# Optimization experiments

Hardware: AMD Instinct MI355X
Metric: run time of the kernel (lower is better)

## Reference

```python
import jax, jax.numpy as jnp
import numpy as np

H = 64  # hidden_dim

def _gru_cell(x, h, Wih, Whh, bih, bhh):
    # PyTorch GRUCell math: gates ordered (r, z, n)
    gi = x @ Wih.T + bih            # [B, 3H]
    gh = h @ Whh.T + bhh            # [B, 3H]
    i_r, i_z, i_n = jnp.split(gi, 3, axis=-1)
    h_r, h_z, h_n = jnp.split(gh, 3, axis=-1)
    r = jax.nn.sigmoid(i_r + h_r)
    z = jax.nn.sigmoid(i_z + h_z)
    n = jnp.tanh(i_n + r * h_n)
    return (1.0 - z) * n + z * h

def setup_inputs() -> dict:
    key = jax.random.key(0)
    ks = jax.random.split(key, 13)
    B, T, D = 128, 512, 512
    x = jax.random.normal(ks[0], (B, T, D), dtype=jnp.float32)
    s = 1.0 / np.sqrt(H)
    def u(k, shape):
        return jax.random.uniform(k, shape, dtype=jnp.float32, minval=-s, maxval=s)
    return {
        "x": x,
        "W0ih": u(ks[1], (3 * H, D)), "W0hh": u(ks[2], (3 * H, H)),
        "b0ih": u(ks[3], (3 * H,)),   "b0hh": u(ks[4], (3 * H,)),
        "W1ih": u(ks[5], (3 * H, H)), "W1hh": u(ks[6], (3 * H, H)),
        "b1ih": u(ks[7], (3 * H,)),   "b1hh": u(ks[8], (3 * H,)),
        "W2ih": u(ks[9], (3 * H, H)), "W2hh": u(ks[10], (3 * H, H)),
        "b2ih": u(ks[11], (3 * H,)),  "b2hh": u(ks[12], (3 * H,)),
    }

def reference(x, W0ih, W0hh, b0ih, b0hh, W1ih, W1hh, b1ih, b1hh,
              W2ih, W2hh, b2ih, b2hh):
    # bContext=True path: per timestep, if the input slice has any nonzero,
    # run the 3 stacked GRU cells and emit h2; else keep states and emit zeros.
    B = x.shape[0]
    h_init = (jnp.zeros((B, H), x.dtype),) * 3

    def step(carry, xt):  # xt: [B, D]
        h0, h1, h2 = carry
        active = jnp.any(xt != 0)
        n0 = _gru_cell(xt, h0, W0ih, W0hh, b0ih, b0hh)
        n1 = _gru_cell(n0, h1, W1ih, W1hh, b1ih, b1hh)
        n2 = _gru_cell(n1, h2, W2ih, W2hh, b2ih, b2hh)
        h0 = jnp.where(active, n0, h0)
        h1 = jnp.where(active, n1, h1)
        h2 = jnp.where(active, n2, h2)
        out = jnp.where(active, h2, jnp.zeros_like(h2))
        return (h0, h1, h2), out

    xs = jnp.swapaxes(x, 0, 1)          # [T, B, D]
    _, outs = jax.lax.scan(step, h_init, xs)  # [T, B, H]
    return jnp.swapaxes(outs, 0, 1)     # [B, T, H]
```

## Files before the change

kernel.cpp:

```cpp
#include <hip/hip_runtime.h>

#define B_ 128
#define T_ 512
#define D_ 512
#define H_ 64
#define N3 192

#if __has_builtin(__builtin_amdgcn_rcpf)
#define RCP(x) __builtin_amdgcn_rcpf(x)
#else
#define RCP(x) (1.0f / (x))
#endif

typedef _Float16 h2v __attribute__((ext_vector_type(2)));
typedef _Float16 f16x8 __attribute__((ext_vector_type(8)));
typedef float f32x4 __attribute__((ext_vector_type(4)));

__device__ __forceinline__ float sigm_f(float x) {
  return RCP(1.0f + __expf(-x));
}
__device__ __forceinline__ float tanh_f(float x) {
  float e = __expf(-2.0f * fabsf(x));
  float t = (1.0f - e) * RCP(1.0f + e);
  return copysignf(t, x);
}

template <int CTRL>
__device__ __forceinline__ float dpp_add(float v) {
  int t = __builtin_amdgcn_update_dpp(0, __float_as_int(v), CTRL, 0xF, 0xF, true);
  return v + __int_as_float(t);
}
__device__ __forceinline__ float red2(float v) { return dpp_add<0xB1>(v); }
__device__ __forceinline__ float red4(float v) {
  v = dpp_add<0xB1>(v);
  v = dpp_add<0x4E>(v);
  return v;
}

__device__ __forceinline__ void dot8reg(const int* w, int4 a, int4 b,
                                        float& s0, float& s1) {
  s0 = __builtin_amdgcn_fdot2(__builtin_bit_cast(h2v, w[0]),
                              __builtin_bit_cast(h2v, a.x), s0, false);
  s1 = __builtin_amdgcn_fdot2(__builtin_bit_cast(h2v, w[1]),
                              __builtin_bit_cast(h2v, a.y), s1, false);
  s0 = __builtin_amdgcn_fdot2(__builtin_bit_cast(h2v, w[2]),
                              __builtin_bit_cast(h2v, a.z), s0, false);
  s1 = __builtin_amdgcn_fdot2(__builtin_bit_cast(h2v, w[3]),
                              __builtin_bit_cast(h2v, a.w), s1, false);
  s0 = __builtin_amdgcn_fdot2(__builtin_bit_cast(h2v, w[4]),
                              __builtin_bit_cast(h2v, b.x), s0, false);
  s1 = __builtin_amdgcn_fdot2(__builtin_bit_cast(h2v, w[5]),
                              __builtin_bit_cast(h2v, b.y), s1, false);
  s0 = __builtin_amdgcn_fdot2(__builtin_bit_cast(h2v, w[6]),
                              __builtin_bit_cast(h2v, b.z), s0, false);
  s1 = __builtin_amdgcn_fdot2(__builtin_bit_cast(h2v, w[7]),
                              __builtin_bit_cast(h2v, b.w), s1, false);
}
__device__ __forceinline__ void dot16reg(const int* w, int4 a, int4 b,
                                         int4 c, int4 d, float& s0, float& s1) {
  dot8reg(w, a, b, s0, s1);
  dot8reg(w + 8, c, d, s0, s1);
}

#define KEEP(x) asm volatile("" : "+v"(x))

#define TICK_BARRIER() asm volatile("s_waitcnt lgkmcnt(0)\ns_barrier" ::: "memory")

__global__ __launch_bounds__(256) void gemm_kernel(
    const float* __restrict__ x,
    const float* __restrict__ w0ih,
    const float* __restrict__ b0ih,
    const float* __restrict__ b0hh,
    float* __restrict__ gi0,
    int* __restrict__ act,
    int t0, int Tc) {
  __shared__ _Float16 Xs[64][72];
  __shared__ _Float16 Ws[64][72];
  __shared__ unsigned char sflag[64];

  const int tid = threadIdx.x;
  const int bid = blockIdx.x;
  const int nt = bid % 3;
  const int mt = bid / 3;
  const int tpc = Tc >> 6;
  const int b  = mt / tpc;
  const int tt = mt % tpc;
  const int c0 = nt * 64;

  const int lane = tid & 63;
  const int wid  = tid >> 6;
  const int wm = (wid >> 1) * 32;
  const int wn = (wid & 1) * 32;
  const int l15 = lane & 15;
  const int l4  = lane >> 4;

  const float* xbase = x + ((size_t)b * T_ + t0 + tt * 64) * D_;
  const float* wbase = w0ih + (size_t)c0 * D_;

  const int srow = tid >> 2;
  const int scg  = (tid & 3) << 4;
  const float* xrow = xbase + (size_t)srow * D_;
  const float* wrow = wbase + (size_t)srow * D_;

  f32x4 acc[2][2];
#pragma unroll
  for (int mi = 0; mi < 2; ++mi)
#pragma unroll
    for (int ni = 0; ni < 2; ++ni) {
      acc[mi][ni].x = 0.f; acc[mi][ni].y = 0.f;
      acc[mi][ni].z = 0.f; acc[mi][ni].w = 0.f;
    }

  bool f = false;

  for (int kt = 0; kt < D_ / 64; ++kt) {
    const int k0 = kt * 64 + scg;
    float4 xa = *(const float4*)&xrow[k0];
    float4 xb = *(const float4*)&xrow[k0 + 4];
    float4 xc = *(const float4*)&xrow[k0 + 8];
    float4 xd = *(const float4*)&xrow[k0 + 12];
    float4 wa = *(const float4*)&wrow[k0];
    float4 wb = *(const float4*)&wrow[k0 + 4];
    float4 wc = *(const float4*)&wrow[k0 + 8];
    float4 wd = *(const float4*)&wrow[k0 + 12];
    f |= (xa.x != 0.f) | (xa.y != 0.f) | (xa.z != 0.f) | (xa.w != 0.f) |
         (xb.x != 0.f) | (xb.y != 0.f) | (xb.z != 0.f) | (xb.w != 0.f) |
         (xc.x != 0.f) | (xc.y != 0.f) | (xc.z != 0.f) | (xc.w != 0.f) |
         (xd.x != 0.f) | (xd.y != 0.f) | (xd.z != 0.f) | (xd.w != 0.f);
    __syncthreads();
    {
      f16x8 p0 = {(_Float16)xa.x, (_Float16)xa.y, (_Float16)xa.z, (_Float16)xa.w,
                  (_Float16)xb.x, (_Float16)xb.y, (_Float16)xb.z, (_Float16)xb.w};
      f16x8 p1 = {(_Float16)xc.x, (_Float16)xc.y, (_Float16)xc.z, (_Float16)xc.w,
                  (_Float16)xd.x, (_Float16)xd.y, (_Float16)xd.z, (_Float16)xd.w};
      *(f16x8*)&Xs[srow][scg] = p0;
      *(f16x8*)&Xs[srow][scg + 8] = p1;
      f16x8 q0 = {(_Float16)wa.x, (_Float16)wa.y, (_Float16)wa.z, (_Float16)wa.w,
                  (_Float16)wb.x, (_Float16)wb.y, (_Float16)wb.z, (_Float16)wb.w};
      f16x8 q1 = {(_Float16)wc.x, (_Float16)wc.y, (_Float16)wc.z, (_Float16)wc.w,
                  (_Float16)wd.x, (_Float16)wd.y, (_Float16)wd.z, (_Float16)wd.w};
      *(f16x8*)&Ws[srow][scg] = q0;
      *(f16x8*)&Ws[srow][scg + 8] = q1;
    }
    __syncthreads();
#pragma unroll
    for (int ks = 0; ks < 2; ++ks) {
      const int kb = ks * 32 + l4 * 8;
      f16x8 a0 = *(const f16x8*)&Xs[wm + l15][kb];
      f16x8 a1 = *(const f16x8*)&Xs[wm + 16 + l15][kb];
      f16x8 b0 = *(const f16x8*)&Ws[wn + l15][kb];
      f16x8 b1 = *(const f16x8*)&Ws[wn + 16 + l15][kb];
      acc[0][0] = __builtin_amdgcn_mfma_f32_16x16x32_f16(a0, b0, acc[0][0], 0, 0, 0);
      acc[0][1] = __builtin_amdgcn_mfma_f32_16x16x32_f16(a0, b1, acc[0][1], 0, 0, 0);
      acc[1][0] = __builtin_amdgcn_mfma_f32_16x16x32_f16(a1, b0, acc[1][0], 0, 0, 0);
      acc[1][1] = __builtin_amdgcn_mfma_f32_16x16x32_f16(a1, b1, acc[1][1], 0, 0, 0);
    }
  }

  const int cA = c0 + wn + l15;
  const int cB = c0 + wn + 16 + l15;
  const float bias0 = b0ih[cA] + ((cA < 128) ? b0hh[cA] : 0.f);
  const float bias1 = b0ih[cB] + ((cB < 128) ? b0hh[cB] : 0.f);
  const size_t rowbase = (size_t)b * Tc + tt * 64;
#pragma unroll
  for (int mi = 0; mi < 2; ++mi)
#pragma unroll
    for (int r = 0; r < 4; ++r) {
      const int m = wm + mi * 16 + l4 * 4 + r;
      float* orow = &gi0[(rowbase + m) * N3 + c0 + wn];
      orow[l15]      = acc[mi][0][r] + bias0;
      orow[16 + l15] = acc[mi][1][r] + bias1;
    }

  if (tid < 64) sflag[tid] = 0;
  __syncthreads();
  if (f) sflag[srow] = 1;
  __syncthreads();
  if (tid < 64 && sflag[tid]) act[t0 + tt * 64 + tid] = 1;
}

__global__ __launch_bounds__(640) void scan_kernel(
    const float* __restrict__ gi0,
    const float* __restrict__ w0hh, const float* __restrict__ w1ih,
    const float* __restrict__ w1hh, const float* __restrict__ w2ih,
    const float* __restrict__ w2hh,
    const float* __restrict__ b0hh, const float* __restrict__ b1ih,
    const float* __restrict__ b1hh, const float* __restrict__ b2ih,
    const float* __restrict__ b2hh,
    const int* __restrict__ act,
    float* __restrict__ hstate,
    float* __restrict__ out,
    int t0, int Tc) {
  const int b   = blockIdx.x;
  const int tid = threadIdx.x;

  __shared__ __align__(16) char s_pad[81920];
  __shared__ __align__(16) _Float16 s_h[3][2][H_];
  __shared__ int s_act[T_];

  if (tid == 0) { volatile char* vp = s_pad; vp[0] = 0; }

  for (int i = tid; i < Tc; i += 640) s_act[i] = act[t0 + i];

  const int grp = (tid < 128) ? 0 : (tid < 384) ? 1 : 2;
  const int lt  = tid - ((grp == 0) ? 0 : (grp == 1) ? 128 : 384);
  const int jj  = (grp == 0) ? (lt >> 1) : (lt >> 2);
  const int gg  = (grp == 0) ? (lt & 1) : (lt & 3);

  if (tid < H_) {
    float v0 = (t0 == 0) ? 0.f : hstate[0 * B_ * H_ + b * H_ + tid];
    float v1 = (t0 == 0) ? 0.f : hstate[1 * B_ * H_ + b * H_ + tid];
    float v2 = (t0 == 0) ? 0.f : hstate[2 * B_ * H_ + b * H_ + tid];
    s_h[0][0][tid] = (_Float16)v0; s_h[0][1][tid] = (_Float16)v0;
    s_h[1][0][tid] = (_Float16)v1; s_h[1][1][tid] = (_Float16)v1;
    s_h[2][0][tid] = (_Float16)v2; s_h[2][1][tid] = (_Float16)v2;
  }
  float hreg = (t0 == 0) ? 0.f : hstate[grp * B_ * H_ + b * H_ + jj];

  int rw0[3][16];
  int rpk[3][8];
  int rhh[3][8];
  if (grp == 0) {
#pragma unroll
    for (int r = 0; r < 3; ++r) {
      const float* src = w0hh + (size_t)(jj + 64 * r) * H_ + 32 * gg;
#pragma unroll
      for (int q = 0; q < 16; ++q) {
        float2 fv = *(const float2*)(src + 2 * q);
        h2v pv = {(_Float16)fv.x, (_Float16)fv.y};
        rw0[r][q] = __builtin_bit_cast(int, pv);
      }
    }
#pragma unroll
    for (int r = 0; r < 3; ++r)
#pragma unroll
      for (int q = 0; q < 16; ++q) KEEP(rw0[r][q]);
  } else {
    const float* ihsrc = (grp == 2) ? w2ih : w1ih;
    const float* hhsrc = (grp == 2) ? w2hh : w1hh;
#pragma unroll
    for (int r = 0; r < 3; ++r) {
      const float* si = ihsrc + (size_t)(jj + 64 * r) * H_ + 16 * gg;
      const float* sh = hhsrc + (size_t)(jj + 64 * r) * H_ + 16 * gg;
#pragma unroll
      for (int q = 0; q < 8; ++q) {
        float2 fi = *(const float2*)(si + 2 * q);
        float2 fh = *(const float2*)(sh + 2 * q);
        h2v pi = {(_Float16)fi.x, (_Float16)fi.y};
        h2v ph = {(_Float16)fh.x, (_Float16)fh.y};
        rpk[r][q] = __builtin_bit_cast(int, pi);
        rhh[r][q] = __builtin_bit_cast(int, ph);
      }
    }
#pragma unroll
    for (int r = 0; r < 3; ++r)
#pragma unroll
      for (int q = 0; q < 8; ++q) { KEEP(rpk[r][q]); KEEP(rhh[r][q]); }
  }

  float bsv[4];
  if (grp == 0) {
    bsv[0] = 0.f; bsv[1] = 0.f; bsv[2] = 0.f;
    bsv[3] = b0hh[jj + 128];
  } else if (grp == 1) {
    bsv[0] = b1ih[jj] + b1hh[jj];
    bsv[1] = b1ih[jj + 64] + b1hh[jj + 64];
    bsv[2] = b1ih[jj + 128]; bsv[3] = b1hh[jj + 128];
  } else {
    bsv[0] = b2ih[jj] + b2hh[jj];
    bsv[1] = b2ih[jj + 64] + b2hh[jj + 64];
    bsv[2] = b2ih[jj + 128]; bsv[3] = b2hh[jj + 128];
  }

  const float* gib = gi0 + (size_t)b * Tc * N3;
  float giR = 0.f, giZ = 0.f, giN = 0.f;
  if (grp == 0) { giR = gib[jj]; giZ = gib[jj + 64]; giN = gib[jj + 128]; }

  __syncthreads();

  for (int i = 0; i < Tc + 2; ++i) {
    const int p = i & 1;
    if (grp == 0) {
      if (i < Tc) {
        const int4* hp = (const int4*)s_h[0][p ^ 1];
        int4 h0s = hp[4 * gg + 0], h1s = hp[4 * gg + 1];
        int4 h2s = hp[4 * gg + 2], h3s = hp[4 * gg + 3];
        float R0 = 0, R1 = 0, Z0 = 0, Z1 = 0, N0 = 0, N1 = 0;
        dot16reg(rw0[0], h0s, h1s, h2s, h3s, R0, R1);
        dot16reg(rw0[1], h0s, h1s, h2s, h3s, Z0, Z1);
        dot16reg(rw0[2], h0s, h1s, h2s, h3s, N0, N1);
        float dR = red2(R0 + R1);
        float dZ = red2(Z0 + Z1);
        float dN = red2(N0 + N1) + bsv[3];
        bool a = (s_act[i] != 0);
        float r = sigm_f(giR + dR);
        float z = sigm_f(giZ + dZ);
        float n = tanh_f(giN + r * dN);
        float hn = (1.0f - z) * n + z * hreg;
        hreg = a ? hn : hreg;
        if (gg == 0) s_h[0][p][jj] = (_Float16)hreg;
        int tn = (i + 1 < Tc) ? i + 1 : i;
        giR = gib[(size_t)tn * N3 + jj];
        giZ = gib[(size_t)tn * N3 + jj + 64];
        giN = gib[(size_t)tn * N3 + jj + 128];
      }
    } else if (grp == 1) {
      if (i >= 1 && i <= Tc) {
        const int4* h0p = (const int4*)s_h[0][p ^ 1];
        const int4* h1p = (const int4*)s_h[1][p ^ 1];
        int4 x0 = h0p[2 * gg], x1 = h0p[2 * gg + 1];
        int4 y0 = h1p[2 * gg], y1 = h1p[2 * gg + 1];
        float vR0 = 0, vR1 = 0, vZ0 = 0, vZ1 = 0;
        float iN0 = 0, iN1 = 0, hN0 = 0, hN1 = 0;
        dot8reg(rpk[0], x0, x1, vR0, vR1);
        dot8reg(rhh[0], y0, y1, vR0, vR1);
        dot8reg(rpk[1], x0, x1, vZ0, vZ1);
        dot8reg(rhh[1], y0, y1, vZ0, vZ1);
        dot8reg(rpk[2], x0, x1, iN0, iN1);
        dot8reg(rhh[2], y0, y1, hN0, hN1);
        float sR = red4(vR0 + vR1) + bsv[0];
        float sZ = red4(vZ0 + vZ1) + bsv[1];
        float iN = red4(iN0 + iN1) + bsv[2];
        float hN = red4(hN0 + hN1) + bsv[3];
        bool a = (s_act[i - 1] != 0);
        float r = sigm_f(sR);
        float z = sigm_f(sZ);
        float n = tanh_f(iN + r * hN);
        float hn = (1.0f - z) * n + z * hreg;
        hreg = a ? hn : hreg;
        if (gg == 0) s_h[1][p][jj] = (_Float16)hreg;
      }
    } else {
      if (i >= 2) {
        const int4* h1p = (const int4*)s_h[1][p ^ 1];
        const int4* h2p = (const int4*)s_h[2][p ^ 1];
        int4 x0 = h1p[2 * gg], x1 = h1p[2 * gg + 1];
        int4 y0 = h2p[2 * gg], y1 = h2p[2 * gg + 1];
        float vR0 = 0, vR1 = 0, vZ0 = 0, vZ1 = 0;
        float iN0 = 0, iN1 = 0, hN0 = 0, hN1 = 0;
        dot8reg(rpk[0], x0, x1, vR0, vR1);
        dot8reg(rhh[0], y0, y1, vR0, vR1);
        dot8reg(rpk[1], x0, x1, vZ0, vZ1);
        dot8reg(rhh[1], y0, y1, vZ0, vZ1);
        dot8reg(rpk[2], x0, x1, iN0, iN1);
        dot8reg(rhh[2], y0, y1, hN0, hN1);
        float sR = red4(vR0 + vR1) + bsv[0];
        float sZ = red4(vZ0 + vZ1) + bsv[1];
        float iN = red4(iN0 + iN1) + bsv[2];
        float hN = red4(hN0 + hN1) + bsv[3];
        bool a = (s_act[i - 2] != 0);
        float r = sigm_f(sR);
        float z = sigm_f(sZ);
        float n = tanh_f(iN + r * hN);
        float hn = (1.0f - z) * n + z * hreg;
        hreg = a ? hn : hreg;
        if (gg == 0) {
          s_h[2][p][jj] = (_Float16)hreg;
          out[((size_t)b * T_ + t0 + (i - 2)) * H_ + jj] = a ? hreg : 0.0f;
        }
      }
    }
    TICK_BARRIER();
  }

  if (gg == 0) hstate[grp * B_ * H_ + b * H_ + jj] = hreg;
}

extern "C" void kernel_launch(void* const* d_in, const int* in_sizes, int n_in,
                              void* d_out, int out_size, void* d_ws, size_t ws_size,
                              hipStream_t stream) {
  const float* x    = (const float*)d_in[0];
  const float* w0ih = (const float*)d_in[1];
  const float* w0hh = (const float*)d_in[2];
  const float* b0ih = (const float*)d_in[3];
  const float* b0hh = (const float*)d_in[4];
  const float* w1ih = (const float*)d_in[5];
  const float* w1hh = (const float*)d_in[6];
  const float* b1ih = (const float*)d_in[7];
  const float* b1hh = (const float*)d_in[8];
  const float* w2ih = (const float*)d_in[9];
  const float* w2hh = (const float*)d_in[10];
  const float* b2ih = (const float*)d_in[11];
  const float* b2hh = (const float*)d_in[12];
  float* out = (float*)d_out;

  char* p = (char*)d_ws;
  int* act      = (int*)p;    p += 4096;
  float* hstate = (float*)p;  p += (size_t)3 * B_ * H_ * 4;
  size_t fixed = (size_t)(p - (char*)d_ws);

  int Tc = T_;
  while (Tc > 64 && fixed + (size_t)B_ * Tc * N3 * 4 > ws_size) Tc >>= 1;
  float* gi0 = (float*)p;

  hipMemsetAsync(act, 0, T_ * sizeof(int), stream);
  for (int t0 = 0; t0 < T_; t0 += Tc) {
    gemm_kernel<<<dim3(B_ * (Tc / 64) * 3), 256, 0, stream>>>(
        x, w0ih, b0ih, b0hh, gi0, act, t0, Tc);
    scan_kernel<<<B_, 640, 0, stream>>>(
        gi0, w0hh, w1ih, w1hh, w2ih, w2hh,
        b0hh, b1ih, b1hh, b2ih, b2hh, act, hstate, out, t0, Tc);
  }
}
```

Baseline: 427.8 us.

## Widen scan kernel to 1024 threads, splitting layer-0 and layer-2 dot products across more lanes

The recurrent scan block grows from 640 to 1024 threads. Layer 0 now uses 4 lanes per hidden unit instead of 2, and layer 2 uses 8 lanes instead of 4, roughly halving each thread's serial fdot2 chain per timestep. Partial sums are combined with an extra DPP reduction step (quad swaps plus half-row mirror). The shared-memory padding that limited blocks per CU is removed. In exchange, each barrier now synchronizes 16 waves instead of 10, there are more reduction shuffles, and register pressure may rise under the larger launch bound.

```diff
diff --git a/kernel.cpp b/kernel.cpp
--- a/kernel.cpp
+++ b/kernel.cpp
@@ -30,13 +30,28 @@
   int t = __builtin_amdgcn_update_dpp(0, __float_as_int(v), CTRL, 0xF, 0xF, true);
   return v + __int_as_float(t);
 }
-__device__ __forceinline__ float red2(float v) { return dpp_add<0xB1>(v); }
 __device__ __forceinline__ float red4(float v) {
   v = dpp_add<0xB1>(v);
   v = dpp_add<0x4E>(v);
   return v;
 }
-
+__device__ __forceinline__ float red8(float v) {
+  v = dpp_add<0xB1>(v);
+  v = dpp_add<0x4E>(v);
+  v = dpp_add<0x141>(v);
+  return v;
+}
+
+__device__ __forceinline__ void dot4acc(int4 w, int4 h, float& s0, float& s1) {
+  s0 = __builtin_amdgcn_fdot2(__builtin_bit_cast(h2v, w.x),
+                              __builtin_bit_cast(h2v, h.x), s0, false);
+  s1 = __builtin_amdgcn_fdot2(__builtin_bit_cast(h2v, w.y),
+                              __builtin_bit_cast(h2v, h.y), s1, false);
+  s0 = __builtin_amdgcn_fdot2(__builtin_bit_cast(h2v, w.z),
+                              __builtin_bit_cast(h2v, h.z), s0, false);
+  s1 = __builtin_amdgcn_fdot2(__builtin_bit_cast(h2v, w.w),
+                              __builtin_bit_cast(h2v, h.w), s1, false);
+}
 __device__ __forceinline__ void dot8reg(const int* w, int4 a, int4 b,
                                         float& s0, float& s1) {
   s0 = __builtin_amdgcn_fdot2(__builtin_bit_cast(h2v, w[0]),
@@ -55,11 +70,6 @@
                               __builtin_bit_cast(h2v, b.z), s0, false);
   s1 = __builtin_amdgcn_fdot2(__builtin_bit_cast(h2v, w[7]),
                               __builtin_bit_cast(h2v, b.w), s1, false);
-}
-__device__ __forceinline__ void dot16reg(const int* w, int4 a, int4 b,
-                                         int4 c, int4 d, float& s0, float& s1) {
-  dot8reg(w, a, b, s0, s1);
-  dot8reg(w + 8, c, d, s0, s1);
 }
 
 #define KEEP(x) asm volatile("" : "+v"(x))
@@ -179,7 +189,7 @@
   if (tid < 64 && sflag[tid]) act[t0 + tt * 64 + tid] = 1;
 }
 
-__global__ __launch_bounds__(640) void scan_kernel(
+__global__ __launch_bounds__(1024) void scan_kernel(
     const float* __restrict__ gi0,
     const float* __restrict__ w0hh, const float* __restrict__ w1ih,
     const float* __restrict__ w1hh, const float* __restrict__ w2ih,
@@ -194,18 +204,15 @@
   const int b   = blockIdx.x;
   const int tid = threadIdx.x;
 
-  __shared__ __align__(16) char s_pad[81920];
   __shared__ __align__(16) _Float16 s_h[3][2][H_];
   __shared__ int s_act[T_];
 
-  if (tid == 0) { volatile char* vp = s_pad; vp[0] = 0; }
-
-  for (int i = tid; i < Tc; i += 640) s_act[i] = act[t0 + i];
-
-  const int grp = (tid < 128) ? 0 : (tid < 384) ? 1 : 2;
-  const int lt  = tid - ((grp == 0) ? 0 : (grp == 1) ? 128 : 384);
-  const int jj  = (grp == 0) ? (lt >> 1) : (lt >> 2);
-  const int gg  = (grp == 0) ? (lt & 1) : (lt & 3);
+  for (int i = tid; i < Tc; i += 1024) s_act[i] = act[t0 + i];
+
+  const int grp = (tid < 256) ? 0 : (tid < 512) ? 1 : 2;
+  const int lt  = tid - ((grp == 0) ? 0 : (grp == 1) ? 256 : 512);
+  const int jj  = (grp == 2) ? (lt >> 3) : (lt >> 2);
+  const int gg  = (grp == 2) ? (lt & 7) : (lt & 3);
 
   if (tid < H_) {
     float v0 = (t0 == 0) ? 0.f : hstate[0 * B_ * H_ + b * H_ + tid];
@@ -217,45 +224,58 @@
   }
   float hreg = (t0 == 0) ? 0.f : hstate[grp * B_ * H_ + b * H_ + jj];
 
-  int rw0[3][16];
-  int rpk[3][8];
+  int rih[3][8];
   int rhh[3][8];
-  if (grp == 0) {
+  int4 sih[3], shh[3];
+  if (grp == 2) {
 #pragma unroll
     for (int r = 0; r < 3; ++r) {
-      const float* src = w0hh + (size_t)(jj + 64 * r) * H_ + 32 * gg;
-#pragma unroll
-      for (int q = 0; q < 16; ++q) {
-        float2 fv = *(const float2*)(src + 2 * q);
-        h2v pv = {(_Float16)fv.x, (_Float16)fv.y};
-        rw0[r][q] = __builtin_bit_cast(int, pv);
-      }
-    }
-#pragma unroll
-    for (int r = 0; r < 3; ++r)
-#pragma unroll
-      for (int q = 0; q < 16; ++q) KEEP(rw0[r][q]);
-  } else {
-    const float* ihsrc = (grp == 2) ? w2ih : w1ih;
-    const float* hhsrc = (grp == 2) ? w2hh : w1hh;
-#pragma unroll
-    for (int r = 0; r < 3; ++r) {
-      const float* si = ihsrc + (size_t)(jj + 64 * r) * H_ + 16 * gg;
-      const float* sh = hhsrc + (size_t)(jj + 64 * r) * H_ + 16 * gg;
-#pragma unroll
-      for (int q = 0; q < 8; ++q) {
+      const float* si = w2ih + (size_t)(jj + 64 * r) * H_ + 8 * gg;
+      const float* sh = w2hh + (size_t)(jj + 64 * r) * H_ + 8 * gg;
+      int tmpi[4], tmph[4];
+#pragma unroll
+      for (int q = 0; q < 4; ++q) {
         float2 fi = *(const float2*)(si + 2 * q);
         float2 fh = *(const float2*)(sh + 2 * q);
         h2v pi = {(_Float16)fi.x, (_Float16)fi.y};
         h2v ph = {(_Float16)fh.x, (_Float16)fh.y};
-        rpk[r][q] = __builtin_bit_cast(int, pi);
-        rhh[r][q] = __builtin_bit_cast(int, ph);
+        tmpi[q] = __builtin_bit_cast(int, pi);
+        tmph[q] = __builtin_bit_cast(int, ph);
+      }
+      sih[r] = make_int4(tmpi[0], tmpi[1], tmpi[2], tmpi[3]);
+      shh[r] = make_int4(tmph[0], tmph[1], tmph[2], tmph[3]);
+    }
+#pragma unroll
+    for (int r = 0; r < 3; ++r) {
+      KEEP(sih[r].x); KEEP(sih[r].y); KEEP(sih[r].z); KEEP(sih[r].w);
+      KEEP(shh[r].x); KEEP(shh[r].y); KEEP(shh[r].z); KEEP(shh[r].w);
+    }
+  } else {
+    const float* ihsrc = (grp == 0) ? w0hh : w1ih;
+    const float* hhsrc = (grp == 0) ? w0hh : w1hh;
+#pragma unroll
+    for (int r = 0; r < 3; ++r) {
+      const float* si = ihsrc + (size_t)(jj + 64 * r) * H_ + 16 * gg;
+      const float* sh = hhsrc + (size_t)(jj + 64 * r) * H_ + 16 * gg;
+#pragma unroll
+      for (int q = 0; q < 8; ++q) {
+        float2 fi = *(const float2*)(si + 2 * q);
+        h2v pi = {(_Float16)fi.x, (_Float16)fi.y};
+        rih[r][q] = __builtin_bit_cast(int, pi);
+        if (grp == 1) {
+          float2 fh = *(const float2*)(sh + 2 * q);
+          h2v ph = {(_Float16)fh.x, (_Float16)fh.y};
+          rhh[r][q] = __builtin_bit_cast(int, ph);
+        }
       }
     }
 #pragma unroll
     for (int r = 0; r < 3; ++r)
 #pragma unroll
-      for (int q = 0; q < 8; ++q) { KEEP(rpk[r][q]); KEEP(rhh[r][q]); }
+      for (int q = 0; q < 8; ++q) {
+        KEEP(rih[r][q]);
+        if (grp == 1) KEEP(rhh[r][q]);
+      }
   }
 
   float bsv[4];
@@ -283,15 +303,14 @@
     if (grp == 0) {
       if (i < Tc) {
         const int4* hp = (const int4*)s_h[0][p ^ 1];
-        int4 h0s = hp[4 * gg + 0], h1s = hp[4 * gg + 1];
-        int4 h2s = hp[4 * gg + 2], h3s = hp[4 * gg + 3];
+        int4 x0 = hp[2 * gg], x1 = hp[2 * gg + 1];
         float R0 = 0, R1 = 0, Z0 = 0, Z1 = 0, N0 = 0, N1 = 0;
-        dot16reg(rw0[0], h0s, h1s, h2s, h3s, R0, R1);
-        dot16reg(rw0[1], h0s, h1s, h2s, h3s, Z0, Z1);
-        dot16reg(rw0[2], h0s, h1s, h2s, h3s, N0, N1);
-        float dR = red2(R0 + R1);
-        float dZ = red2(Z0 + Z1);
-        float dN = red2(N0 + N1) + bsv[3];
+        dot8reg(rih[0], x0, x1, R0, R1);
+        dot8reg(rih[1], x0, x1, Z0, Z1);
+        dot8reg(rih[2], x0, x1, N0, N1);
+        float dR = red4(R0 + R1);
+        float dZ = red4(Z0 + Z1);
+        float dN = red4(N0 + N1) + bsv[3];
         bool a = (s_act[i] != 0);
         float r = sigm_f(giR + dR);
         float z = sigm_f(giZ + dZ);
@@ -312,11 +331,11 @@
         int4 y0 = h1p[2 * gg], y1 = h1p[2 * gg + 1];
         float vR0 = 0, vR1 = 0, vZ0 = 0, vZ1 = 0;
         float iN0 = 0, iN1 = 0, hN0 = 0, hN1 = 0;
-        dot8reg(rpk[0], x0, x1, vR0, vR1);
+        dot8reg(rih[0], x0, x1, vR0, vR1);
         dot8reg(rhh[0], y0, y1, vR0, vR1);
-        dot8reg(rpk[1], x0, x1, vZ0, vZ1);
+        dot8reg(rih[1], x0, x1, vZ0, vZ1);
         dot8reg(rhh[1], y0, y1, vZ0, vZ1);
-        dot8reg(rpk[2], x0, x1, iN0, iN1);
+        dot8reg(rih[2], x0, x1, iN0, iN1);
         dot8reg(rhh[2], y0, y1, hN0, hN1);
         float sR = red4(vR0 + vR1) + bsv[0];
         float sZ = red4(vZ0 + vZ1) + bsv[1];
@@ -334,20 +353,20 @@
       if (i >= 2) {
         const int4* h1p = (const int4*)s_h[1][p ^ 1];
         const int4* h2p = (const int4*)s_h[2][p ^ 1];
-        int4 x0 = h1p[2 * gg], x1 = h1p[2 * gg + 1];
-        int4 y0 = h2p[2 * gg], y1 = h2p[2 * gg + 1];
+        int4 x0 = h1p[gg];
+        int4 y0 = h2p[gg];
         float vR0 = 0, vR1 = 0, vZ0 = 0, vZ1 = 0;
         float iN0 = 0, iN1 = 0, hN0 = 0, hN1 = 0;
-        dot8reg(rpk[0], x0, x1, vR0, vR1);
-        dot8reg(rhh[0], y0, y1, vR0, vR1);
-        dot8reg(rpk[1], x0, x1, vZ0, vZ1);
-        dot8reg(rhh[1], y0, y1, vZ0, vZ1);
-        dot8reg(rpk[2], x0, x1, iN0, iN1);
-        dot8reg(rhh[2], y0, y1, hN0, hN1);
-        float sR = red4(vR0 + vR1) + bsv[0];
-        float sZ = red4(vZ0 + vZ1) + bsv[1];
-        float iN = red4(iN0 + iN1) + bsv[2];
-        float hN = red4(hN0 + hN1) + bsv[3];
+        dot4acc(sih[0], x0, vR0, vR1);
+        dot4acc(shh[0], y0, vR0, vR1);
+        dot4acc(sih[1], x0, vZ0, vZ1);
+        dot4acc(shh[1], y0, vZ0, vZ1);
+        dot4acc(sih[2], x0, iN0, iN1);
+        dot4acc(shh[2], y0, hN0, hN1);
+        float sR = red8(vR0 + vR1) + bsv[0];
+        float sZ = red8(vZ0 + vZ1) + bsv[1];
+        float iN = red8(iN0 + iN1) + bsv[2];
+        float hN = red8(hN0 + hN1) + bsv[3];
         bool a = (s_act[i - 2] != 0);
         float r = sigm_f(sR);
         float z = sigm_f(sZ);
@@ -397,7 +416,7 @@
   for (int t0 = 0; t0 < T_; t0 += Tc) {
     gemm_kernel<<<dim3(B_ * (Tc / 64) * 3), 256, 0, stream>>>(
         x, w0ih, b0ih, b0hh, gi0, act, t0, Tc);
-    scan_kernel<<<B_, 640, 0, stream>>>(
+    scan_kernel<<<B_, 1024, 0, stream>>>(
         gi0, w0hh, w1ih, w1hh, w2ih, w2hh,
         b0hh, b1ih, b1hh, b2ih, b2hh, act, hstate, out, t0, Tc);
   }
```

After: 461.4 us. 7.9% more time.
